# Kernel optimization log

Hardware: AMD Instinct MI355X
Metric: run time of the kernel (lower is better)

Reference implementation:

```python
import jax, jax.numpy as jnp
import numpy as np

B, C, H, W = 1, 448, 64, 64
K, M, PAD, STRIDE = 7, 7, 3, 1
CG = C // K          # key/query channels (KeyQueryMap divides by k) = 64
GP_HID = int(0.5 * CG)  # geometry prior hidden channels = 32
K2 = K * K
CENTER = K2 // 2


def conv1x1(x, w, b):
    # x: (B, Cin, H, W), w: (Cout, Cin), b: (Cout,)
    return jnp.einsum('bchw,oc->bohw', x, w) + b[None, :, None, None]


def unfold(x):
    # torch.nn.Unfold(K, dilation=1, padding=PAD, stride=STRIDE)
    # output layout: (B, Cin*K2, L) with dim1 index = c*K2 + (di*K + dj)
    Bc, Cc, Hc, Wc = x.shape
    xp = jnp.pad(x, ((0, 0), (0, 0), (PAD, PAD), (PAD, PAD)))
    Ho = (Hc + 2 * PAD - K) // STRIDE + 1
    Wo = (Wc + 2 * PAD - K) // STRIDE + 1
    patches = [xp[:, :, di:di + Ho * STRIDE:STRIDE, dj:dj + Wo * STRIDE:STRIDE]
               for di in range(K) for dj in range(K)]
    u = jnp.stack(patches, axis=2)  # (B, Cc, K2, Ho, Wo)
    return u.reshape(Bc, Cc * K2, Ho * Wo), Ho, Wo


def geometry_prior(gp_w1, gp_b1, gp_w2, gp_b2):
    ar = jnp.arange(-(K // 2), K // 2 + 1, dtype=jnp.float32)   # -3..3
    x_pos = jnp.broadcast_to(ar[None, :], (K, K))
    y_pos = jnp.broadcast_to(ar[::-1][:, None], (K, K))          # 3..-3 down rows
    pos = jnp.stack([x_pos, y_pos], axis=0)[None]                # (1, 2, K, K)
    h = jax.nn.relu(conv1x1(pos, gp_w1, gp_b1))
    out = conv1x1(h, gp_w2, gp_b2)                               # (1, CG, K, K)
    return out.reshape(1, CG, 1, K2)


def setup_inputs() -> dict:
    key = jax.random.key(0)
    ks = jax.random.split(key, 12)
    def lin(k, cout, cin):
        return jax.random.normal(k, (cout, cin), jnp.float32) / np.sqrt(cin)
    inp = {
        'x': jax.random.normal(ks[0], (B, C, H, W), jnp.float32),
        'Wk': lin(ks[1], CG, C), 'bk': jnp.zeros((CG,), jnp.float32),
        'Wq': lin(ks[2], CG, C), 'bq': jnp.zeros((CG,), jnp.float32),
        'gp_w1': lin(ks[3], GP_HID, 2), 'gp_b1': jax.random.normal(ks[4], (GP_HID,), jnp.float32) * 0.01,
        'gp_w2': lin(ks[5], CG, GP_HID), 'gp_b2': jax.random.normal(ks[6], (CG,), jnp.float32) * 0.01,
        'Wf': lin(ks[7], C, C), 'bf': jnp.zeros((C,), jnp.float32),
    }
    return inp


def reference(x, Wk, bk, Wq, bq, gp_w1, gp_b1, gp_w2, gp_b2, Wf, bf):
    gpk = geometry_prior(gp_w1, gp_b1, gp_w2, gp_b2)        # (1, CG, 1, K2)
    km = conv1x1(x, Wk, bk)                                  # (B, CG, H, W)
    qm = conv1x1(x, Wq, bq)
    ku, Ho, Wo = unfold(km)
    L = Ho * Wo
    ku = ku.reshape(B, CG, L, K2)   # same row-major semantics as torch .view
    qu, _, _ = unfold(qm)
    qu = qu.reshape(B, CG, L, K2)
    ak = ku * qu[:, :, :, CENTER:CENTER + 1]                 # (B, CG, L, K2)
    ck = jax.nn.softmax(ak + gpk, axis=-1)                   # (B, CG, L, K2)
    xu, _, _ = unfold(x)
    xu = xu.reshape(B, M, C // M, L, K2)                     # (B, M, CG, L, K2)
    # ck broadcasts over the M axis (valid since B == 1); sum over window dim
    pre = jnp.einsum('bglp,bmglp->bmgl', ck, xu).reshape(B, C, Ho, Wo)
    return conv1x1(pre, Wf, bf)
```

## Files before the change

### kernel.cpp

```cpp
#include <hip/hip_runtime.h>
#include <hip/hip_bf16.h>

#define CC   448
#define CGC  64
#define MMM  7
#define HWSZ 4096
#define KK2  49
#define GPH  32

typedef __attribute__((ext_vector_type(8))) short   short8;
typedef __attribute__((ext_vector_type(4))) float   f32x4;
typedef __attribute__((ext_vector_type(4))) unsigned short us4;

__device__ __forceinline__ unsigned short f2b(float f) {
    union { __hip_bfloat16 h; unsigned short u; } cv;
    cv.h = __float2bfloat16(f);
    return cv.u;
}

__global__ __launch_bounds__(256) void kq_mfma(
    const float* __restrict__ x,
    const float* __restrict__ Wk, const float* __restrict__ bk,
    const float* __restrict__ Wq, const float* __restrict__ bq,
    float* __restrict__ km, float* __restrict__ qm)
{
    __shared__ unsigned short As[4096];
    __shared__ unsigned short Bs[1024];

    const int tid  = threadIdx.x;
    const int nT   = blockIdx.x * 32;
    const int lane = tid & 63;
    const int wid  = tid >> 6;
    const int wm   = wid * 32;
    const int l15  = lane & 15;
    const int l4   = lane >> 4;

    const int ar = tid >> 3;
    const int ak = tid & 7;
    const int bkr = tid >> 3;
    const int bn4 = tid & 7;

    f32x4 acc[2][2];
    #pragma unroll
    for (int i = 0; i < 2; ++i)
        #pragma unroll
        for (int j = 0; j < 2; ++j)
            acc[i][j] = (f32x4){0.f, 0.f, 0.f, 0.f};

    float4 a0 = *(const float4*)(Wk + (size_t)ar * CC + ak * 4);
    float4 a1 = *(const float4*)(Wk + (size_t)(ar + 32) * CC + ak * 4);
    float4 a2 = *(const float4*)(Wq + (size_t)ar * CC + ak * 4);
    float4 a3 = *(const float4*)(Wq + (size_t)(ar + 32) * CC + ak * 4);
    float4 b0 = *(const float4*)(x + (size_t)bkr * HWSZ + nT + bn4 * 4);

    for (int kt = 0; kt < 14; ++kt) {
        {
            int kg = ak >> 1, jo = (ak & 1) * 4;
            us4 w;
            w = (us4){ f2b(a0.x), f2b(a0.y), f2b(a0.z), f2b(a0.w) };
            *(us4*)&As[kg * 1024 + (ar +  0) * 8 + jo] = w;
            w = (us4){ f2b(a1.x), f2b(a1.y), f2b(a1.z), f2b(a1.w) };
            *(us4*)&As[kg * 1024 + (ar + 32) * 8 + jo] = w;
            w = (us4){ f2b(a2.x), f2b(a2.y), f2b(a2.z), f2b(a2.w) };
            *(us4*)&As[kg * 1024 + (ar + 64) * 8 + jo] = w;
            w = (us4){ f2b(a3.x), f2b(a3.y), f2b(a3.z), f2b(a3.w) };
            *(us4*)&As[kg * 1024 + (ar + 96) * 8 + jo] = w;
            int base = (bkr >> 3) * 256 + bn4 * 32 + (bkr & 7);
            Bs[base]      = f2b(b0.x);
            Bs[base + 8]  = f2b(b0.y);
            Bs[base + 16] = f2b(b0.z);
            Bs[base + 24] = f2b(b0.w);
        }
        if (kt < 13) {
            int ko = (kt + 1) * 32;
            a0 = *(const float4*)(Wk + (size_t)ar * CC + ko + ak * 4);
            a1 = *(const float4*)(Wk + (size_t)(ar + 32) * CC + ko + ak * 4);
            a2 = *(const float4*)(Wq + (size_t)ar * CC + ko + ak * 4);
            a3 = *(const float4*)(Wq + (size_t)(ar + 32) * CC + ko + ak * 4);
            b0 = *(const float4*)(x + (size_t)(ko + bkr) * HWSZ + nT + bn4 * 4);
        }
        __syncthreads();
        short8 fa0 = *(short8*)&As[l4 * 1024 + (wm + l15) * 8];
        short8 fa1 = *(short8*)&As[l4 * 1024 + (wm + 16 + l15) * 8];
        short8 fb0 = *(short8*)&Bs[l4 * 256 + l15 * 8];
        short8 fb1 = *(short8*)&Bs[l4 * 256 + (16 + l15) * 8];
        acc[0][0] = __builtin_amdgcn_mfma_f32_16x16x32_bf16(fa0, fb0, acc[0][0], 0, 0, 0);
        acc[0][1] = __builtin_amdgcn_mfma_f32_16x16x32_bf16(fa0, fb1, acc[0][1], 0, 0, 0);
        acc[1][0] = __builtin_amdgcn_mfma_f32_16x16x32_bf16(fa1, fb0, acc[1][0], 0, 0, 0);
        acc[1][1] = __builtin_amdgcn_mfma_f32_16x16x32_bf16(fa1, fb1, acc[1][1], 0, 0, 0);
        __syncthreads();
    }
    const bool isK = (wid < 2);
    float*       Cd   = isK ? km : qm;
    const float* bias = isK ? bk : bq;
    const int rbase = (wm & 63);
    #pragma unroll
    for (int wm2 = 0; wm2 < 2; ++wm2)
        #pragma unroll
        for (int wn2 = 0; wn2 < 2; ++wn2)
            #pragma unroll
            for (int r = 0; r < 4; ++r) {
                int row = rbase + wm2 * 16 + l4 * 4 + r;
                int col = nT + wn2 * 16 + l15;
                Cd[(size_t)row * HWSZ + col] = acc[wm2][wn2][r] + bias[row];
            }
}

__global__ __launch_bounds__(256) void fconv_mfma(
    const float* __restrict__ pre,
    const float* __restrict__ Wf, const float* __restrict__ bfv,
    float* __restrict__ out)
{
    __shared__ unsigned short As[2048];
    __shared__ unsigned short Bs[1024];

    const int tid  = threadIdx.x;
    const int nT   = blockIdx.x * 32;
    const int oT   = blockIdx.y * 64;
    const int lane = tid & 63;
    const int wid  = tid >> 6;
    const int l15  = lane & 15;
    const int l4   = lane >> 4;

    const int ar = tid >> 3;
    const int ak = tid & 7;
    const int bkr = tid >> 3;
    const int bn4 = tid & 7;

    const float* __restrict__ A = Wf + (size_t)oT * CC;

    f32x4 acc[2];
    acc[0] = (f32x4){0.f, 0.f, 0.f, 0.f};
    acc[1] = (f32x4){0.f, 0.f, 0.f, 0.f};

    float4 a0 = *(const float4*)(A + (size_t)ar * CC + ak * 4);
    float4 a1 = *(const float4*)(A + (size_t)(ar + 32) * CC + ak * 4);
    float4 b0 = *(const float4*)(pre + (size_t)bkr * HWSZ + nT + bn4 * 4);

    for (int kt = 0; kt < 14; ++kt) {
        {
            int kg = ak >> 1, jo = (ak & 1) * 4;
            us4 w;
            w = (us4){ f2b(a0.x), f2b(a0.y), f2b(a0.z), f2b(a0.w) };
            *(us4*)&As[kg * 512 + (ar +  0) * 8 + jo] = w;
            w = (us4){ f2b(a1.x), f2b(a1.y), f2b(a1.z), f2b(a1.w) };
            *(us4*)&As[kg * 512 + (ar + 32) * 8 + jo] = w;
            int base = (bkr >> 3) * 256 + bn4 * 32 + (bkr & 7);
            Bs[base]      = f2b(b0.x);
            Bs[base + 8]  = f2b(b0.y);
            Bs[base + 16] = f2b(b0.z);
            Bs[base + 24] = f2b(b0.w);
        }
        if (kt < 13) {
            int ko = (kt + 1) * 32;
            a0 = *(const float4*)(A + (size_t)ar * CC + ko + ak * 4);
            a1 = *(const float4*)(A + (size_t)(ar + 32) * CC + ko + ak * 4);
            b0 = *(const float4*)(pre + (size_t)(ko + bkr) * HWSZ + nT + bn4 * 4);
        }
        __syncthreads();
        short8 fa  = *(short8*)&As[l4 * 512 + (wid * 16 + l15) * 8];
        short8 fb0 = *(short8*)&Bs[l4 * 256 + l15 * 8];
        short8 fb1 = *(short8*)&Bs[l4 * 256 + (16 + l15) * 8];
        acc[0] = __builtin_amdgcn_mfma_f32_16x16x32_bf16(fa, fb0, acc[0], 0, 0, 0);
        acc[1] = __builtin_amdgcn_mfma_f32_16x16x32_bf16(fa, fb1, acc[1], 0, 0, 0);
        __syncthreads();
    }
    #pragma unroll
    for (int wn2 = 0; wn2 < 2; ++wn2)
        #pragma unroll
        for (int r = 0; r < 4; ++r) {
            int row = oT + wid * 16 + l4 * 4 + r;
            int col = nT + wn2 * 16 + l15;
            out[(size_t)row * HWSZ + col] = acc[wn2][r] + bfv[row];
        }
}

#define GLO 196
#define GHI 260
#define XWORDS (GLO + HWSZ + GHI)

__device__ __forceinline__ int win_off_global(int n, bool& ok) {
    int p  = n >> 12;
    int l  = n & 4095;
    int di = (p * 37) >> 8;
    int dj = p - di * 7;
    int i  = (l >> 6) + di - 3;
    int j  = (l & 63) + dj - 3;
    ok = ((unsigned)i < 64u) && ((unsigned)j < 64u);
    return i * 64 + j;
}

__global__ __launch_bounds__(256) void attn_kernel(
    const float* __restrict__ km, const float* __restrict__ qm,
    const float* __restrict__ x,
    const float* __restrict__ gw1, const float* __restrict__ gb1,
    const float* __restrict__ gw2, const float* __restrict__ gb2,
    float* __restrict__ pre)
{
    __shared__ float klin[XWORDS];
    __shared__ float xlin[XWORDS];
    __shared__ float gpk_s[KK2];
    const int tid = threadIdx.x;
    const int g   = blockIdx.y;
    const int lp  = blockIdx.x * 256 + tid;

    if (tid < 114) {
        float4 z = {0.f, 0.f, 0.f, 0.f};
        int w = (tid < 49) ? tid * 4 : (GLO + HWSZ + (tid - 49) * 4);
        *(float4*)&klin[w] = z;
        *(float4*)&xlin[w] = z;
    }
    {
        const float4* km4 = (const float4*)(km + (size_t)g * HWSZ);
        #pragma unroll
        for (int i = 0; i < 4; ++i) {
            int idx = tid + i * 256;
            *(float4*)&klin[GLO + idx * 4] = km4[idx];
        }
    }
    if (tid < KK2) {
        int di = tid / 7, dj = tid - di * 7;
        float xp = (float)(dj - 3);
        float yp = (float)(3 - di);
        float acc = gb2[g];
        #pragma unroll
        for (int j = 0; j < GPH; ++j) {
            float h = gw1[j * 2 + 0] * xp + gw1[j * 2 + 1] * yp + gb1[j];
            h = fmaxf(h, 0.f);
            acc = fmaf(gw2[g * GPH + j], h, acc);
        }
        gpk_s[tid] = acc;
    }

    float qc;
    { bool ok; int o = win_off_global(lp * KK2 + 24, ok); qc = ok ? qm[(size_t)g * HWSZ + o] : 0.f; }

    const int n0 = lp * KK2;
    const int p0 = n0 >> 12;
    const int l0 = n0 & 4095;
    const int ts = ((p0 + 1) << 12) - n0;
    const int di0 = (p0 * 37) >> 8, dj0 = p0 - di0 * 7;
    const int p1  = p0 + 1;
    const int di1 = (p1 * 37) >> 8, dj1 = p1 - di1 * 7;
    const int djm3_0 = dj0 - 3, djm3_1 = dj1 - 3;
    const int B0 = GLO + l0 + (di0 - 3) * 64 + djm3_0;
    const int B1 = GLO + l0 - 4096 + (di1 - 3) * 64 + djm3_1;

    float4 xr0, xr1, xr2, xr3;
    {
        const float4* xg4 = (const float4*)(x + (size_t)g * HWSZ);
        xr0 = xg4[tid]; xr1 = xg4[tid + 256]; xr2 = xg4[tid + 512]; xr3 = xg4[tid + 768];
    }
    __syncthreads();

    float a[KK2];
    float mx = -1e30f;
    #pragma unroll
    for (int t = 0; t < KK2; ++t) {
        bool s1 = (t >= ts);
        int base = s1 ? B1 : B0;
        float kv = klin[base + t];
        int jj = ((l0 + t) & 63) + (s1 ? djm3_1 : djm3_0);
        kv = ((unsigned)jj < 64u) ? kv : 0.f;
        float av = fmaf(kv, qc, gpk_s[t]);
        a[t] = av;
        mx = fmaxf(mx, av);
    }
    float d = 0.f;
    #pragma unroll
    for (int t = 0; t < KK2; ++t) {
        float e = __expf(a[t] - mx);
        d += e;
        bool s1 = (t >= ts);
        int jj = ((l0 + t) & 63) + (s1 ? djm3_1 : djm3_0);
        a[t] = ((unsigned)jj < 64u) ? e : 0.f;
    }
    const float inv = 1.f / d;

    #pragma unroll 1
    for (int m = 0; m < MMM; ++m) {
        __syncthreads();
        *(float4*)&xlin[GLO + tid * 4]          = xr0;
        *(float4*)&xlin[GLO + (tid + 256) * 4]  = xr1;
        *(float4*)&xlin[GLO + (tid + 512) * 4]  = xr2;
        *(float4*)&xlin[GLO + (tid + 768) * 4]  = xr3;
        if (m < MMM - 1) {
            const float4* xg4 = (const float4*)(x + (size_t)((m + 1) * CGC + g) * HWSZ);
            xr0 = xg4[tid]; xr1 = xg4[tid + 256]; xr2 = xg4[tid + 512]; xr3 = xg4[tid + 768];
        }
        __syncthreads();
        float acc = 0.f;
        #pragma unroll
        for (int t = 0; t < KK2; ++t) {
            int base = (t >= ts) ? B1 : B0;
            acc = fmaf(a[t], xlin[base + t], acc);
        }
        pre[(size_t)(m * CGC + g) * HWSZ + lp] = acc * inv;
    }
}

extern "C" void kernel_launch(void* const* d_in, const int* in_sizes, int n_in,
                              void* d_out, int out_size, void* d_ws, size_t ws_size,
                              hipStream_t stream) {
    const float* x   = (const float*)d_in[0];
    const float* Wk  = (const float*)d_in[1];
    const float* bk  = (const float*)d_in[2];
    const float* Wq  = (const float*)d_in[3];
    const float* bq  = (const float*)d_in[4];
    const float* gw1 = (const float*)d_in[5];
    const float* gb1 = (const float*)d_in[6];
    const float* gw2 = (const float*)d_in[7];
    const float* gb2 = (const float*)d_in[8];
    const float* Wf  = (const float*)d_in[9];
    const float* bfv = (const float*)d_in[10];
    float* out = (float*)d_out;

    float* km  = (float*)d_ws;
    float* qm  = km + CGC * HWSZ;
    float* pre = qm + CGC * HWSZ;

    kq_mfma    <<<dim3(128),     256, 0, stream>>>(x, Wk, bk, Wq, bq, km, qm);
    attn_kernel<<<dim3(16, CGC), 256, 0, stream>>>(km, qm, x, gw1, gb1, gw2, gb2, pre);
    fconv_mfma <<<dim3(128, 7),  256, 0, stream>>>(pre, Wf, bfv, out);
}
```

Measured before the change: 115.9 us.

## Split attention window across two thread halves and reorder GEMM prefetch barriers

The attention kernel now runs 512 threads per block. Each pixel's 49-tap window is split between two wave groups that combine max, sum and partial dot products through shared memory. This halves the per-thread logit array, which should cut register pressure and raise occupancy, at the cost of extra barriers and shared-memory reductions. In both MFMA GEMM kernels the barrier now sits before the next-tile global prefetch rather than after it, so the loads are issued alongside the MFMA work.

```diff
diff --git a/kernel.cpp b/kernel.cpp
--- a/kernel.cpp
+++ b/kernel.cpp
@@ -71,6 +71,7 @@
             Bs[base + 16] = f2b(b0.z);
             Bs[base + 24] = f2b(b0.w);
         }
+        __syncthreads();
         if (kt < 13) {
             int ko = (kt + 1) * 32;
             a0 = *(const float4*)(Wk + (size_t)ar * CC + ko + ak * 4);
@@ -79,7 +80,6 @@
             a3 = *(const float4*)(Wq + (size_t)(ar + 32) * CC + ko + ak * 4);
             b0 = *(const float4*)(x + (size_t)(ko + bkr) * HWSZ + nT + bn4 * 4);
         }
-        __syncthreads();
         short8 fa0 = *(short8*)&As[l4 * 1024 + (wm + l15) * 8];
         short8 fa1 = *(short8*)&As[l4 * 1024 + (wm + 16 + l15) * 8];
         short8 fb0 = *(short8*)&Bs[l4 * 256 + l15 * 8];
@@ -151,13 +151,13 @@
             Bs[base + 16] = f2b(b0.z);
             Bs[base + 24] = f2b(b0.w);
         }
+        __syncthreads();
         if (kt < 13) {
             int ko = (kt + 1) * 32;
             a0 = *(const float4*)(A + (size_t)ar * CC + ko + ak * 4);
             a1 = *(const float4*)(A + (size_t)(ar + 32) * CC + ko + ak * 4);
             b0 = *(const float4*)(pre + (size_t)(ko + bkr) * HWSZ + nT + bn4 * 4);
         }
-        __syncthreads();
         short8 fa  = *(short8*)&As[l4 * 512 + (wid * 16 + l15) * 8];
         short8 fb0 = *(short8*)&Bs[l4 * 256 + l15 * 8];
         short8 fb1 = *(short8*)&Bs[l4 * 256 + (16 + l15) * 8];
@@ -190,7 +190,7 @@
     return i * 64 + j;
 }
 
-__global__ __launch_bounds__(256) void attn_kernel(
+__global__ __launch_bounds__(512) void attn_kernel(
     const float* __restrict__ km, const float* __restrict__ qm,
     const float* __restrict__ x,
     const float* __restrict__ gw1, const float* __restrict__ gb1,
@@ -200,9 +200,15 @@
     __shared__ float klin[XWORDS];
     __shared__ float xlin[XWORDS];
     __shared__ float gpk_s[KK2];
-    const int tid = threadIdx.x;
-    const int g   = blockIdx.y;
-    const int lp  = blockIdx.x * 256 + tid;
+    __shared__ float red[2][256];
+
+    const int tid  = threadIdx.x;
+    const int lane = tid & 63;
+    const int wid  = tid >> 6;
+    const int half = wid >> 2;
+    const int lpi  = (wid & 3) * 64 + lane;
+    const int g    = blockIdx.y;
+    const int lp   = blockIdx.x * 256 + lpi;
 
     if (tid < 114) {
         float4 z = {0.f, 0.f, 0.f, 0.f};
@@ -212,11 +218,8 @@
     }
     {
         const float4* km4 = (const float4*)(km + (size_t)g * HWSZ);
-        #pragma unroll
-        for (int i = 0; i < 4; ++i) {
-            int idx = tid + i * 256;
-            *(float4*)&klin[GLO + idx * 4] = km4[idx];
-        }
+        *(float4*)&klin[GLO + tid * 4]         = km4[tid];
+        *(float4*)&klin[GLO + (tid + 512) * 4] = km4[tid + 512];
     }
     if (tid < KK2) {
         int di = tid / 7, dj = tid - di * 7;
@@ -246,56 +249,83 @@
     const int B0 = GLO + l0 + (di0 - 3) * 64 + djm3_0;
     const int B1 = GLO + l0 - 4096 + (di1 - 3) * 64 + djm3_1;
 
-    float4 xr0, xr1, xr2, xr3;
+    float4 xr0, xr1;
     {
         const float4* xg4 = (const float4*)(x + (size_t)g * HWSZ);
-        xr0 = xg4[tid]; xr1 = xg4[tid + 256]; xr2 = xg4[tid + 512]; xr3 = xg4[tid + 768];
+        xr0 = xg4[tid]; xr1 = xg4[tid + 512];
     }
     __syncthreads();
 
-    float a[KK2];
+    float w[25];
     float mx = -1e30f;
-    #pragma unroll
-    for (int t = 0; t < KK2; ++t) {
-        bool s1 = (t >= ts);
-        int base = s1 ? B1 : B0;
-        float kv = klin[base + t];
-        int jj = ((l0 + t) & 63) + (s1 ? djm3_1 : djm3_0);
-        kv = ((unsigned)jj < 64u) ? kv : 0.f;
-        float av = fmaf(kv, qc, gpk_s[t]);
-        a[t] = av;
-        mx = fmaxf(mx, av);
-    }
+#define LOGIT(T, I) { \
+        bool s1 = ((T) >= ts); \
+        int base = s1 ? B1 : B0; \
+        float kv = klin[base + (T)]; \
+        int jj = ((l0 + (T)) & 63) + (s1 ? djm3_1 : djm3_0); \
+        kv = ((unsigned)jj < 64u) ? kv : 0.f; \
+        float av = fmaf(kv, qc, gpk_s[(T)]); \
+        w[(I)] = av; mx = fmaxf(mx, av); }
+    if (half == 0) {
+        #pragma unroll
+        for (int t = 0; t < 25; ++t) LOGIT(t, t)
+    } else {
+        #pragma unroll
+        for (int t = 25; t < 49; ++t) LOGIT(t, t - 25)
+    }
+#undef LOGIT
+    red[half][lpi] = mx;
+    __syncthreads();
+    mx = fmaxf(mx, red[1 - half][lpi]);
+
     float d = 0.f;
-    #pragma unroll
-    for (int t = 0; t < KK2; ++t) {
-        float e = __expf(a[t] - mx);
-        d += e;
-        bool s1 = (t >= ts);
-        int jj = ((l0 + t) & 63) + (s1 ? djm3_1 : djm3_0);
-        a[t] = ((unsigned)jj < 64u) ? e : 0.f;
-    }
-    const float inv = 1.f / d;
+#define EXPW(T, I) { \
+        float e = __expf(w[(I)] - mx); \
+        d += e; \
+        bool s1 = ((T) >= ts); \
+        int jj = ((l0 + (T)) & 63) + (s1 ? djm3_1 : djm3_0); \
+        w[(I)] = ((unsigned)jj < 64u) ? e : 0.f; }
+    if (half == 0) {
+        #pragma unroll
+        for (int t = 0; t < 25; ++t) EXPW(t, t)
+    } else {
+        #pragma unroll
+        for (int t = 25; t < 49; ++t) EXPW(t, t - 25)
+    }
+#undef EXPW
+    __syncthreads();
+    red[half][lpi] = d;
+    __syncthreads();
+    const float inv = 1.f / (d + red[1 - half][lpi]);
 
     #pragma unroll 1
     for (int m = 0; m < MMM; ++m) {
         __syncthreads();
-        *(float4*)&xlin[GLO + tid * 4]          = xr0;
-        *(float4*)&xlin[GLO + (tid + 256) * 4]  = xr1;
-        *(float4*)&xlin[GLO + (tid + 512) * 4]  = xr2;
-        *(float4*)&xlin[GLO + (tid + 768) * 4]  = xr3;
+        *(float4*)&xlin[GLO + tid * 4]         = xr0;
+        *(float4*)&xlin[GLO + (tid + 512) * 4] = xr1;
+        __syncthreads();
         if (m < MMM - 1) {
             const float4* xg4 = (const float4*)(x + (size_t)((m + 1) * CGC + g) * HWSZ);
-            xr0 = xg4[tid]; xr1 = xg4[tid + 256]; xr2 = xg4[tid + 512]; xr3 = xg4[tid + 768];
-        }
-        __syncthreads();
-        float acc = 0.f;
-        #pragma unroll
-        for (int t = 0; t < KK2; ++t) {
-            int base = (t >= ts) ? B1 : B0;
-            acc = fmaf(a[t], xlin[base + t], acc);
-        }
-        pre[(size_t)(m * CGC + g) * HWSZ + lp] = acc * inv;
+            xr0 = xg4[tid]; xr1 = xg4[tid + 512];
+        }
+        float part = 0.f;
+        if (half == 0) {
+            #pragma unroll
+            for (int t = 0; t < 25; ++t) {
+                int base = (t >= ts) ? B1 : B0;
+                part = fmaf(w[t], xlin[base + t], part);
+            }
+        } else {
+            #pragma unroll
+            for (int t = 25; t < 49; ++t) {
+                int base = (t >= ts) ? B1 : B0;
+                part = fmaf(w[t - 25], xlin[base + t], part);
+            }
+        }
+        if (half == 1) red[1][lpi] = part;
+        __syncthreads();
+        if (half == 0)
+            pre[(size_t)(m * CGC + g) * HWSZ + lp] = (part + red[1][lpi]) * inv;
     }
 }
 
@@ -320,6 +350,6 @@
     float* pre = qm + CGC * HWSZ;
 
     kq_mfma    <<<dim3(128),     256, 0, stream>>>(x, Wk, bk, Wq, bq, km, qm);
-    attn_kernel<<<dim3(16, CGC), 256, 0, stream>>>(km, qm, x, gw1, gb1, gw2, gb2, pre);
+    attn_kernel<<<dim3(16, CGC), 512, 0, stream>>>(km, qm, x, gw1, gb1, gw2, gb2, pre);
     fconv_mfma <<<dim3(128, 7),  256, 0, stream>>>(pre, Wf, bfv, out);
 }
```

After: 133.1 us. +14.8%, slower.
